# Optimization experiments

Measured on AMD Instinct MI355X. Metric: run time of the kernel, lower is better.

Reference implementation:

```python
import jax, jax.numpy as jnp
import numpy as np

B, N, E, H = 2, 4096, 1024, 16
HD = E // H                      # head_dim = 64
R = 8                            # LoRA rank
LORA_SCALE = 16.0 / R            # alpha / r = 2.0
BUCKET_SIZES = (256, 64, 16)


def setup_inputs() -> dict:
    key = jax.random.key(0)
    ks = jax.random.split(key, 24)
    inp = {"x": jax.random.normal(ks[0], (B, N, E), jnp.float32)}
    inp["wb_coarse"] = jax.random.randint(ks[1], (B, N), 0, 16)
    inp["wb_mid"] = jax.random.randint(ks[2], (B, N), 0, 64)
    inp["wb_fine"] = jax.random.randint(ks[3], (B, N), 0, 256)
    i = 4
    for name in ("q", "k", "v", "o"):
        inp[f"W{name}"] = jax.random.normal(ks[i], (E, E), jnp.float32) / np.sqrt(E); i += 1
        inp[f"b{name}"] = jax.random.normal(ks[i], (E,), jnp.float32) * 0.01; i += 1
        inp[f"A{name}"] = jax.random.normal(ks[i], (R, E), jnp.float32) / np.sqrt(E); i += 1
        inp[f"B{name}"] = jax.random.normal(ks[i], (E, R), jnp.float32) * 0.01; i += 1
    return inp


def _lora(x, W, b, A, Bm):
    # F.linear(x, W, b) + scale * x @ A.T @ B.T   (dropout=0 in eval)
    return x @ W.T + b + LORA_SCALE * ((x @ A.T) @ Bm.T)


def _chunked_attn(q, k, v, bidx, C):
    # q,k,v: [BH, N, D]; bidx: [BH, N] int; C: chunk size (divides N)
    BH, Nn, D = q.shape
    sidx = jnp.argsort(bidx, axis=1)
    uidx = jnp.argsort(sidx, axis=1)
    g = lambda t, i: jnp.take_along_axis(t, i[..., None], axis=1)
    qs, ks_, vs = g(q, sidx), g(k, sidx), g(v, sidx)
    nc = Nn // C
    qs = qs.reshape(BH, nc, C, D)
    ks_ = ks_.reshape(BH, nc, C, D)
    vs = vs.reshape(BH, nc, C, D)
    # previous chunk (look-back of one chunk); chunk 0 has no previous -> masked
    k_prev = jnp.concatenate([jnp.zeros_like(ks_[:, :1]), ks_[:, :-1]], axis=1)
    v_prev = jnp.concatenate([jnp.zeros_like(vs[:, :1]), vs[:, :-1]], axis=1)
    k_cat = jnp.concatenate([k_prev, ks_], axis=2)   # [BH, nc, 2C, D]
    v_cat = jnp.concatenate([v_prev, vs], axis=2)
    scores = jnp.einsum('bncd,bnkd->bnck', qs, k_cat) / jnp.sqrt(jnp.asarray(D, qs.dtype))
    # mask look-back keys for chunk 0 (torch path attends only within chunk 0)
    chunk_ids = jnp.arange(nc)[:, None, None]        # [nc,1,1]
    key_pos = jnp.arange(2 * C)[None, None, :]       # [1,1,2C]
    neg = jnp.finfo(scores.dtype).min
    scores = jnp.where((chunk_ids == 0) & (key_pos < C), neg, scores)
    attn = jax.nn.softmax(scores, axis=-1)
    out = jnp.einsum('bnck,bnkd->bncd', attn, v_cat).reshape(BH, Nn, D)
    return jnp.take_along_axis(out, uidx[..., None], axis=1)


def reference(x, wb_coarse, wb_mid, wb_fine,
              Wq, bq, Aq, Bq, Wk, bk, Ak, Bk,
              Wv, bv, Av, Bv, Wo, bo, Ao, Bo):
    q = _lora(x, Wq, bq, Aq, Bq)
    k = _lora(x, Wk, bk, Ak, Bk)
    v = _lora(x, Wv, bv, Av, Bv)
    to_heads = lambda t: t.reshape(B, N, H, HD).transpose(0, 2, 1, 3).reshape(B * H, N, HD)
    qh, kh, vh = to_heads(q), to_heads(k), to_heads(v)
    expand = lambda w: jnp.broadcast_to(w[:, None, :], (B, H, N)).reshape(B * H, N)
    wbs = (expand(wb_coarse), expand(wb_mid), expand(wb_fine))
    outs = (_chunked_attn(qh, kh, vh, wbs[0], BUCKET_SIZES[0])
            + _chunked_attn(qh, kh, vh, wbs[1], BUCKET_SIZES[1])
            + _chunked_attn(qh, kh, vh, wbs[2], BUCKET_SIZES[2])) / 3.0
    outs = outs.reshape(B, H, N, HD).transpose(0, 2, 1, 3).reshape(B, N, E)
    return _lora(outs, Wo, bo, Ao, Bo)
```

## Files before the change

kernel.cpp:

```cpp
#include <hip/hip_runtime.h>
#include <cstdint>
#include <cstddef>

#define BDIM 2
#define NTOK 4096
#define EDIM 1024
#define HEADS 16
#define HDIM 64
#define MROWS (BDIM * NTOK)

typedef unsigned short u16;
typedef __attribute__((ext_vector_type(8))) short bf16x8;
typedef __attribute__((ext_vector_type(8))) unsigned short u16x8;
typedef __attribute__((ext_vector_type(4))) float f32x4;

#define MFMA(a, b, c) __builtin_amdgcn_mfma_f32_16x16x32_bf16(a, b, c, 0, 0, 0)
#define BAR() asm volatile("s_barrier" ::: "memory")
#define SETPRIO(p) __builtin_amdgcn_s_setprio(p)

__device__ inline void split2(float x, u16& h, u16& l) {
    union { float f; unsigned u; } a;
    a.f = x;
    unsigned uh = a.u + 0x7fff + ((a.u >> 16) & 1);
    h = (u16)(uh >> 16);
    union { unsigned u; float f; } hf; hf.u = (unsigned)h << 16;
    a.f = x - hf.f;
    unsigned ul = a.u + 0x7fff + ((a.u >> 16) & 1);
    l = (u16)(ul >> 16);
}

__device__ inline u16 bf16rne(float x) {
    union { float f; unsigned u; } a; a.f = x;
    unsigned r = a.u + 0x7fff + ((a.u >> 16) & 1);
    return (u16)(r >> 16);
}

#define GLL(gp, lp) __builtin_amdgcn_global_load_lds( \
    (const __attribute__((address_space(1))) unsigned*)(gp), \
    (__attribute__((address_space(3))) unsigned*)(lp), 16, 0, 0)

__global__ __launch_bounds__(256) void prep_kernel(
    const float* __restrict__ x, u16* __restrict__ xh, u16* __restrict__ xl,
    const int* __restrict__ w0, const int* __restrict__ w1,
    const int* __restrict__ w2, int* __restrict__ sidx,
    const float* __restrict__ W0, const float* __restrict__ A0, const float* __restrict__ B0,
    const float* __restrict__ W1, const float* __restrict__ A1, const float* __restrict__ B1,
    const float* __restrict__ W2, const float* __restrict__ A2, const float* __restrict__ B2,
    const float* __restrict__ W3, const float* __restrict__ A3, const float* __restrict__ B3,
    u16* __restrict__ dh0, u16* __restrict__ dl0,
    u16* __restrict__ dh1, u16* __restrict__ dl1,
    u16* __restrict__ dh2, u16* __restrict__ dl2,
    u16* __restrict__ dh3, u16* __restrict__ dl3)
{
    __shared__ int sb[NTOK];
    __shared__ int cnt[32][256];
    __shared__ int gb[256];
    int bid = blockIdx.x;
    int t = threadIdx.x;

    if (bid < 6) {
        int by = bid >> 1, bx = bid & 1;
        const int* srcs[3] = {w0, w1, w2};
        const int* w = srcs[by] + bx * NTOK;
        int* outp = sidx + ((int)by * BDIM + (int)bx) * NTOK;

        for (int i = t; i < NTOK; i += 256) sb[i] = w[i];
        for (int i = t; i < 32 * 256; i += 256) ((int*)cnt)[i] = 0;
        __syncthreads();

        int g = t >> 3;
#pragma unroll
        for (int e = 0; e < 16; ++e)
            atomicAdd(&cnt[g][sb[g * 128 + (t & 7) + 8 * e]], 1);
        __syncthreads();

        int run = 0;
#pragma unroll
        for (int gg = 0; gg < 32; ++gg) {
            int c = cnt[gg][t];
            cnt[gg][t] = run;
            run += c;
        }
        gb[t] = run;
        __syncthreads();
        if (t == 0) {
            int acc = 0;
            for (int v = 0; v < 256; ++v) { int c = gb[v]; gb[v] = acc; acc += c; }
        }
        __syncthreads();
        for (int i = t; i < 32 * 256; i += 256) {
            int v = i & 255, gg = i >> 8;
            cnt[gg][v] += gb[v];
        }
        __syncthreads();

        if (t < 32) {
            int base = t * 128;
            for (int e = 0; e < 128; ++e) {
                int v = sb[base + e];
                int p = cnt[t][v]++;
                outp[p] = base + e;
            }
        }
    } else if (bid < 8198) {
        int idx = (bid - 6) * 256 + t;
        float4 v = ((const float4*)x)[idx];
        ushort4 h, l;
        split2(v.x, h.x, l.x);
        split2(v.y, h.y, l.y);
        split2(v.z, h.z, l.z);
        split2(v.w, h.w, l.w);
        ((ushort4*)xh)[idx] = h;
        ((ushort4*)xl)[idx] = l;
    } else {
        int wid = bid - 8198;
        int s = wid >> 12, bx = wid & 4095;
        const float* W = (s == 0) ? W0 : (s == 1) ? W1 : (s == 2) ? W2 : W3;
        const float* A = (s == 0) ? A0 : (s == 1) ? A1 : (s == 2) ? A2 : A3;
        const float* Bm = (s == 0) ? B0 : (s == 1) ? B1 : (s == 2) ? B2 : B3;
        u16* dh = (s == 0) ? dh0 : (s == 1) ? dh1 : (s == 2) ? dh2 : dh3;
        u16* dl = (s == 0) ? dl0 : (s == 1) ? dl1 : (s == 2) ? dl2 : dl3;

        int idx = bx * 256 + t;
        int o = idx >> 10, i = idx & 1023;
        float sum = 0.f;
#pragma unroll
        for (int r = 0; r < 8; ++r) sum += Bm[o * 8 + r] * A[r * 1024 + i];
        float w = W[idx] + 2.0f * sum;
        u16 h, l;
        split2(w, h, l);
        dh[idx] = h; dl[idx] = l;
    }
}

__global__ __launch_bounds__(256) void sumsplit3_kernel(
    const float* __restrict__ A, const float* __restrict__ B,
    const float* __restrict__ Cc, u16* __restrict__ dh, u16* __restrict__ dl)
{
    int idx = blockIdx.x * 256 + threadIdx.x;
    float4 a = ((const float4*)A)[idx];
    float4 b = ((const float4*)B)[idx];
    float4 c = ((const float4*)Cc)[idx];
    float v[4] = {(a.x + b.x) + c.x, (a.y + b.y) + c.y,
                  (a.z + b.z) + c.z, (a.w + b.w) + c.w};
    ushort4 h, l;
    split2(v[0], h.x, l.x);
    split2(v[1], h.y, l.y);
    split2(v[2], h.z, l.z);
    split2(v[3], h.w, l.w);
    ((ushort4*)dh)[idx] = h;
    ((ushort4*)dl)[idx] = l;
}

__global__ __launch_bounds__(256) void split_kernel(
    const float* __restrict__ src, u16* __restrict__ dh, u16* __restrict__ dl)
{
    int idx = blockIdx.x * 256 + threadIdx.x;
    float4 v = ((const float4*)src)[idx];
    ushort4 h, l;
    split2(v.x, h.x, l.x);
    split2(v.y, h.y, l.y);
    split2(v.z, h.z, l.z);
    split2(v.w, h.w, l.w);
    ((ushort4*)dh)[idx] = h;
    ((ushort4*)dl)[idx] = l;
}

__global__ __launch_bounds__(512, 2) void gemm_qkv_kernel(
    const u16* __restrict__ Xh, const u16* __restrict__ Xl,
    const u16* __restrict__ Wh, const u16* __restrict__ Wl,
    const u16* __restrict__ Wvh,
    const float* __restrict__ bq, const float* __restrict__ bk,
    const float* __restrict__ bv,
    u16* __restrict__ qh, u16* __restrict__ ql,
    u16* __restrict__ kh, u16* __restrict__ kl, u16* __restrict__ vh)
{
    __shared__ __align__(16) unsigned char smem[147456];
    u16* lds = (u16*)smem;
    int t = threadIdx.x;
    int lane = t & 63, wave = t >> 6;
    int bid = blockIdx.x;

    if (bid < 256) {
        int wg = (bid & 7) * 32 + (bid >> 3);
        int bx = wg & 7, by = wg >> 3;
        int m0 = by * 256, nc0 = bx * 128;

        int lrow = lane & 15, lq = lane >> 4;
        size_t aoff = (size_t)(m0 + wave * 32 + lrow) * EDIM + lq * 8;
        size_t boff = (size_t)(nc0 + wave * 16 + lrow) * EDIM + lq * 8;
        int slabA = wave * 2;
        int sA0 = (wave >> 1) * 4;
        int sB0 = (wave & 1) * 4;
        f32x4 acc[4][4] = {};

#pragma unroll
        for (int tt = 0; tt < 2; ++tt) {
            u16* sbuf = lds + tt * 12288;
            int kk = tt * 32;
            GLL(Xh + aoff + kk,             sbuf + (slabA + 0) * 512);
            GLL(Xh + aoff + kk + 16 * EDIM, sbuf + (slabA + 1) * 512);
            GLL(Wvh + boff + kk,            sbuf + 8192 + wave * 512);
        }
        asm volatile("s_waitcnt vmcnt(3)" ::: "memory");
        BAR();

        for (int t32 = 0; t32 < 32; ++t32) {
            u16* rb = lds + (t32 % 3) * 12288;
            u16* sbuf = lds + ((t32 + 2) % 3) * 12288;
            bool pf = (t32 + 2) < 32;
            int kn = (t32 + 2) * 32;

            bf16x8 bhf[4];
#pragma unroll
            for (int j = 0; j < 4; ++j)
                bhf[j] = *(const bf16x8*)(rb + 8192 + (sB0 + j) * 512 + lane * 8);
            bf16x8 a0 = *(const bf16x8*)(rb + (sA0 + 0) * 512 + lane * 8);
            bf16x8 a1 = *(const bf16x8*)(rb + (sA0 + 1) * 512 + lane * 8);
            if (pf) {
                GLL(Xh + aoff + kn,             sbuf + (slabA + 0) * 512);
                GLL(Xh + aoff + kn + 16 * EDIM, sbuf + (slabA + 1) * 512);
            }
            BAR();
            SETPRIO(1);
#pragma unroll
            for (int j = 0; j < 4; ++j) {
                acc[0][j] = MFMA(a0, bhf[j], acc[0][j]);
                acc[1][j] = MFMA(a1, bhf[j], acc[1][j]);
            }
            SETPRIO(0);
            BAR();

            bf16x8 a2 = *(const bf16x8*)(rb + (sA0 + 2) * 512 + lane * 8);
            bf16x8 a3 = *(const bf16x8*)(rb + (sA0 + 3) * 512 + lane * 8);
            if (pf) GLL(Wvh + boff + kn, sbuf + 8192 + wave * 512);
            BAR();
            SETPRIO(1);
#pragma unroll
            for (int j = 0; j < 4; ++j) {
                acc[2][j] = MFMA(a2, bhf[j], acc[2][j]);
                acc[3][j] = MFMA(a3, bhf[j], acc[3][j]);
            }
            SETPRIO(0);
            if (pf) asm volatile("s_waitcnt vmcnt(3)" ::: "memory");
            else    asm volatile("s_waitcnt vmcnt(0)" ::: "memory");
            BAR();
        }

        int wm = (wave >> 1) * 64, wn = (wave & 1) * 64;
        int q4 = lane >> 4, l16 = lane & 15;
        int cb = nc0 + wn;
        float bj[4];
#pragma unroll
        for (int j = 0; j < 4; ++j) bj[j] = bv[cb + j * 16 + l16];
        float* repw = (float*)smem + wave * 2176;
        int r8 = lane >> 3, c8 = lane & 7;
#pragma unroll
        for (int gph = 0; gph < 2; ++gph) {
#pragma unroll
            for (int ii = 0; ii < 2; ++ii)
#pragma unroll
                for (int j = 0; j < 4; ++j)
#pragma unroll
                    for (int r = 0; r < 4; ++r)
                        repw[(ii * 16 + q4 * 4 + r) * 68 + j * 16 + l16] =
                            acc[gph * 2 + ii][j][r] + bj[j];
#pragma unroll
            for (int rg = 0; rg < 4; ++rg) {
                int lr = rg * 8 + r8;
                float4 f0 = *(float4*)(repw + lr * 68 + c8 * 8);
                float4 f1 = *(float4*)(repw + lr * 68 + c8 * 8 + 4);
                float fa[8] = {f0.x, f0.y, f0.z, f0.w, f1.x, f1.y, f1.z, f1.w};
                size_t off = (size_t)(m0 + wm + gph * 32 + lr) * EDIM + cb + c8 * 8;
                u16x8 hv;
#pragma unroll
                for (int e = 0; e < 8; ++e) hv[e] = bf16rne(fa[e]);
                *(u16x8*)(vh + off) = hv;
            }
        }
    } else {
        const int PA_h = 0, PA_l = 8192, PB_h = 16384, PB_l = 20480;
        int qidx = bid - 256;
        int wg = (qidx & 7) * 64 + (qidx >> 3);
        int bx = wg & 15, by = wg >> 4;
        int m0 = by * 256, n0 = bx * 128;

        int lrow = lane & 15, lq = lane >> 4;
        size_t aoff = (size_t)(m0 + wave * 32 + lrow) * EDIM + lq * 8;
        size_t boff = (size_t)(n0 + wave * 16 + lrow) * EDIM + lq * 8;
        int slabA = wave * 2;
        int sA0 = (wave >> 1) * 4;
        int sB0 = (wave & 1) * 4;
        f32x4 acc[4][4] = {};

#pragma unroll
        for (int tt = 0; tt < 2; ++tt) {
            u16* sbuf = lds + tt * 24576;
            int kk = tt * 32;
            GLL(Xh + aoff + kk,             sbuf + PA_h + (slabA + 0) * 512);
            GLL(Xh + aoff + kk + 16 * EDIM, sbuf + PA_h + (slabA + 1) * 512);
            GLL(Xl + aoff + kk,             sbuf + PA_l + (slabA + 0) * 512);
            GLL(Xl + aoff + kk + 16 * EDIM, sbuf + PA_l + (slabA + 1) * 512);
            GLL(Wh + boff + kk, sbuf + PB_h + wave * 512);
            GLL(Wl + boff + kk, sbuf + PB_l + wave * 512);
        }
        asm volatile("s_waitcnt vmcnt(6)" ::: "memory");
        BAR();

        for (int t32 = 0; t32 < 32; ++t32) {
            u16* rb = lds + (t32 % 3) * 24576;
            u16* sbuf = lds + ((t32 + 2) % 3) * 24576;
            bool pf = (t32 + 2) < 32;
            int kn = (t32 + 2) * 32;
            bf16x8 bhf[4], blf[4];
#pragma unroll
            for (int p = 0; p < 4; ++p) {
                if (p == 0) {
#pragma unroll
                    for (int j = 0; j < 4; ++j) {
                        bhf[j] = *(const bf16x8*)(rb + PB_h + (sB0 + j) * 512 + lane * 8);
                        blf[j] = *(const bf16x8*)(rb + PB_l + (sB0 + j) * 512 + lane * 8);
                    }
                }
                bf16x8 aph = *(const bf16x8*)(rb + PA_h + (sA0 + p) * 512 + lane * 8);
                bf16x8 apl = *(const bf16x8*)(rb + PA_l + (sA0 + p) * 512 + lane * 8);
                if (pf) {
                    if (p == 0) {
                        GLL(Xh + aoff + kn,             sbuf + PA_h + (slabA + 0) * 512);
                        GLL(Xh + aoff + kn + 16 * EDIM, sbuf + PA_h + (slabA + 1) * 512);
                    } else if (p == 1) {
                        GLL(Xl + aoff + kn,             sbuf + PA_l + (slabA + 0) * 512);
                        GLL(Xl + aoff + kn + 16 * EDIM, sbuf + PA_l + (slabA + 1) * 512);
                    } else if (p == 2) {
                        GLL(Wh + boff + kn, sbuf + PB_h + wave * 512);
                        GLL(Wl + boff + kn, sbuf + PB_l + wave * 512);
                    }
                }
                BAR();
                SETPRIO(1);
#pragma unroll
                for (int j = 0; j < 4; ++j) {
                    acc[p][j] = MFMA(aph, bhf[j], acc[p][j]);
                    acc[p][j] = MFMA(aph, blf[j], acc[p][j]);
                    acc[p][j] = MFMA(apl, bhf[j], acc[p][j]);
                }
                SETPRIO(0);
                if (p == 3) {
                    if (pf) asm volatile("s_waitcnt vmcnt(6)" ::: "memory");
                    else    asm volatile("s_waitcnt vmcnt(0)" ::: "memory");
                }
                BAR();
            }
        }

        int proj = n0 >> 10;
        const float* bias = proj ? bk : bq;
        u16* ohp = proj ? kh : qh;
        u16* olp = proj ? kl : ql;
        int wm = (wave >> 1) * 64, wn = (wave & 1) * 64;
        int q4 = lane >> 4, l16 = lane & 15;
        int cb = (n0 & 1023) + wn;
        float bj[4];
#pragma unroll
        for (int j = 0; j < 4; ++j) bj[j] = bias[cb + j * 16 + l16];
        float* repw = (float*)smem + wave * 2176;
        int r8 = lane >> 3, c8 = lane & 7;
#pragma unroll
        for (int gph = 0; gph < 2; ++gph) {
#pragma unroll
            for (int ii = 0; ii < 2; ++ii)
#pragma unroll
                for (int j = 0; j < 4; ++j)
#pragma unroll
                    for (int r = 0; r < 4; ++r)
                        repw[(ii * 16 + q4 * 4 + r) * 68 + j * 16 + l16] =
                            acc[gph * 2 + ii][j][r] + bj[j];
#pragma unroll
            for (int rg = 0; rg < 4; ++rg) {
                int lr = rg * 8 + r8;
                float4 f0 = *(float4*)(repw + lr * 68 + c8 * 8);
                float4 f1 = *(float4*)(repw + lr * 68 + c8 * 8 + 4);
                float fa[8] = {f0.x, f0.y, f0.z, f0.w, f1.x, f1.y, f1.z, f1.w};
                size_t off = (size_t)(m0 + wm + gph * 32 + lr) * EDIM + cb + c8 * 8;
                u16x8 hv, lv;
#pragma unroll
                for (int e = 0; e < 8; ++e) {
                    float v = fa[e];
                    if (proj == 0) v *= 0.125f;
                    u16 hh, ll;
                    split2(v, hh, ll);
                    hv[e] = hh; lv[e] = ll;
                }
                *(u16x8*)(ohp + off) = hv;
                *(u16x8*)(olp + off) = lv;
            }
        }
    }
}

__global__ __launch_bounds__(512, 2) void gemm_o_kernel(
    const u16* __restrict__ Xh, const u16* __restrict__ Xl,
    const u16* __restrict__ Wh, const u16* __restrict__ Wl,
    const float* __restrict__ bias, float* __restrict__ Y)
{
    __shared__ __align__(16) unsigned char smem[147456];
    u16* lds = (u16*)smem;
    const int PA_h = 0, PA_l = 8192, PB_h = 16384, PB_l = 20480;

    int t = threadIdx.x;
    int lane = t & 63, wave = t >> 6;
    int bid = blockIdx.x;
    int wg = (bid & 7) * 32 + (bid >> 3);
    int bx = wg & 7, by = wg >> 3;
    int m0 = by * 256, n0 = bx * 128;

    int lrow = lane & 15, lq = lane >> 4;
    size_t aoff = (size_t)(m0 + wave * 32 + lrow) * EDIM + lq * 8;
    size_t boff = (size_t)(n0 + wave * 16 + lrow) * EDIM + lq * 8;
    int slabA = wave * 2;
    int sA0 = (wave >> 1) * 4;
    int sB0 = (wave & 1) * 4;
    f32x4 acc[4][4] = {};

#pragma unroll
    for (int tt = 0; tt < 2; ++tt) {
        u16* sbuf = lds + tt * 24576;
        int kk = tt * 32;
        GLL(Xh + aoff + kk,             sbuf + PA_h + (slabA + 0) * 512);
        GLL(Xh + aoff + kk + 16 * EDIM, sbuf + PA_h + (slabA + 1) * 512);
        GLL(Xl + aoff + kk,             sbuf + PA_l + (slabA + 0) * 512);
        GLL(Xl + aoff + kk + 16 * EDIM, sbuf + PA_l + (slabA + 1) * 512);
        GLL(Wh + boff + kk, sbuf + PB_h + wave * 512);
        GLL(Wl + boff + kk, sbuf + PB_l + wave * 512);
    }
    asm volatile("s_waitcnt vmcnt(6)" ::: "memory");
    BAR();

    for (int t32 = 0; t32 < 32; ++t32) {
        u16* rb = lds + (t32 % 3) * 24576;
        u16* sbuf = lds + ((t32 + 2) % 3) * 24576;
        bool pf = (t32 + 2) < 32;
        int kn = (t32 + 2) * 32;
        bf16x8 bhf[4], blf[4];
#pragma unroll
        for (int p = 0; p < 4; ++p) {
            if (p == 0) {
#pragma unroll
                for (int j = 0; j < 4; ++j) {
                    bhf[j] = *(const bf16x8*)(rb + PB_h + (sB0 + j) * 512 + lane * 8);
                    blf[j] = *(const bf16x8*)(rb + PB_l + (sB0 + j) * 512 + lane * 8);
                }
            }
            bf16x8 aph = *(const bf16x8*)(rb + PA_h + (sA0 + p) * 512 + lane * 8);
            bf16x8 apl = *(const bf16x8*)(rb + PA_l + (sA0 + p) * 512 + lane * 8);
            if (pf) {
                if (p == 0) {
                    GLL(Xh + aoff + kn,             sbuf + PA_h + (slabA + 0) * 512);
                    GLL(Xh + aoff + kn + 16 * EDIM, sbuf + PA_h + (slabA + 1) * 512);
                } else if (p == 1) {
                    GLL(Xl + aoff + kn,             sbuf + PA_l + (slabA + 0) * 512);
                    GLL(Xl + aoff + kn + 16 * EDIM, sbuf + PA_l + (slabA + 1) * 512);
                } else if (p == 2) {
                    GLL(Wh + boff + kn, sbuf + PB_h + wave * 512);
                    GLL(Wl + boff + kn, sbuf + PB_l + wave * 512);
                }
            }
            BAR();
            SETPRIO(1);
#pragma unroll
            for (int j = 0; j < 4; ++j) {
                acc[p][j] = MFMA(aph, bhf[j], acc[p][j]);
                acc[p][j] = MFMA(aph, blf[j], acc[p][j]);
                acc[p][j] = MFMA(apl, bhf[j], acc[p][j]);
            }
            SETPRIO(0);
            if (p == 3) {
                if (pf) asm volatile("s_waitcnt vmcnt(6)" ::: "memory");
                else    asm volatile("s_waitcnt vmcnt(0)" ::: "memory");
            }
            BAR();
        }
    }

    int wm = (wave >> 1) * 64, wn = (wave & 1) * 64;
    int col_in = lane & 15, rquad = lane >> 4;
#pragma unroll
    for (int j = 0; j < 4; ++j) {
        int col = n0 + wn + j * 16 + col_in;
        float bvv = bias[col];
#pragma unroll
        for (int i = 0; i < 4; ++i) {
            int mbase = m0 + wm + i * 16 + rquad * 4;
#pragma unroll
            for (int r = 0; r < 4; ++r)
                Y[(size_t)(mbase + r) * EDIM + col] = acc[i][j][r] + bvv;
        }
    }
}

template <int MODE>
__global__ __launch_bounds__(256, 3) void attn_mfma_kernel(
    const u16* __restrict__ Qh, const u16* __restrict__ Ql,
    const u16* __restrict__ Kh, const u16* __restrict__ Kl,
    const u16* __restrict__ Vh, const int* __restrict__ sidx_base, int zofs,
    float* __restrict__ out0, float* __restrict__ out1, float* __restrict__ out2,
    u16* __restrict__ osh, u16* __restrict__ osl)
{
    __shared__ u16 KfH[2][4096], KfL[2][4096];
    __shared__ u16 VL[64 * 72];
    __shared__ u16 PbH[4 * 2 * 16 * 40];

    int bx_, bh_, bz_;
    if (MODE == 0 && gridDim.z == 3) {
        int lid = blockIdx.x + (blockIdx.y << 5) + (blockIdx.z << 10);
        int xcd = lid & 7, j = lid >> 3;
        bh_ = xcd + 8 * (j / 96);
        int rem = j % 96;
        bz_ = rem >> 5;
        bx_ = rem & 31;
    } else {
        bx_ = blockIdx.x; bh_ = blockIdx.y; bz_ = blockIdx.z;
    }

    int sidx_i = bz_ + zofs;
    int lgC = 8 - 2 * sidx_i;
    const int* sxb = sidx_base + sidx_i * BDIM * NTOK;
    float* out = (sidx_i == 0) ? out0 : (sidx_i == 1) ? out1 : out2;

    int t = threadIdx.x;
    int lane = t & 63, wave = t >> 6;
    int quad = lane >> 4, l16 = lane & 15;
    int b = bh_ >> 4, h = bh_ & 15;
    int p0 = bx_ * 128;
    sxb += b * NTOK;

    int ptile[2], ws_[2], we_[2];
    bf16x8 qhf[2][2], qlf[2][2];
#pragma unroll
    for (int tq = 0; tq < 2; ++tq) {
        ptile[tq] = p0 + wave * 32 + tq * 16;
        int c = ptile[tq] >> lgC;
        ws_[tq] = (c > 0) ? (c - 1) << lgC : 0;
        we_[tq] = (c + 1) << lgC;
        int qrow = sxb[ptile[tq] + l16];
        size_t rb = (size_t)(b * NTOK + qrow) * EDIM + h * HDIM + quad * 8;
#pragma unroll
        for (int kk = 0; kk < 2; ++kk) {
            qhf[tq][kk] = *(const bf16x8*)(Qh + rb + kk * 32);
            qlf[tq][kk] = *(const bf16x8*)(Ql + rb + kk * 32);
        }
    }

    f32x4 oacc[2][4] = {};
    float lpart[2][4] = {};
    float mrun[2] = {-1e30f, -1e30f};

    int c0 = p0 >> lgC, c1 = (p0 + 127) >> lgC;
    int kmin = (c0 > 0) ? (c0 - 1) << lgC : 0;
    int kmax = (c1 + 1) << lgC;
    int nsteps = (kmax - kmin + 63) >> 6;

    {
        int tok = sxb[min(kmin + wave * 16 + l16, NTOK - 1)];
        size_t rb = (size_t)(b * NTOK + tok) * EDIM + h * HDIM + quad * 8;
        GLL(Kh + rb,      &KfH[0][(wave * 2 + 0) * 512]);
        GLL(Kh + rb + 32, &KfH[0][(wave * 2 + 1) * 512]);
        GLL(Kl + rb,      &KfL[0][(wave * 2 + 0) * 512]);
        GLL(Kl + rb + 32, &KfL[0][(wave * 2 + 1) * 512]);
        bf16x8 vreg[2];
#pragma unroll
        for (int it = 0; it < 2; ++it) {
            int c = it * 256 + t;
            int key = c & 63, dg = c >> 6;
            int tok2 = sxb[min(kmin + key, NTOK - 1)];
            vreg[it] = *(const bf16x8*)(Vh + (size_t)(b * NTOK + tok2) * EDIM + h * HDIM + dg * 8);
        }
#pragma unroll
        for (int it = 0; it < 2; ++it) {
            int c = it * 256 + t;
            int key = c & 63, dg = c >> 6;
#pragma unroll
            for (int e = 0; e < 8; ++e)
                VL[(dg * 8 + e) * 72 + key] = (u16)vreg[it][e];
        }
        asm volatile("s_waitcnt vmcnt(0)" ::: "memory");
        __syncthreads();
    }

    int pb = 0;
    for (int s = 0; s < nsteps; ++s) {
        int ks = kmin + s * 64;
        int nk = min(64, kmax - ks);
        bool pf = (s + 1) < nsteps;
        bf16x8 vreg[2];
        if (pf) {
            int ks2 = ks + 64;
            int tok = sxb[min(ks2 + wave * 16 + l16, NTOK - 1)];
            size_t rb = (size_t)(b * NTOK + tok) * EDIM + h * HDIM + quad * 8;
            GLL(Kh + rb,      &KfH[pb ^ 1][(wave * 2 + 0) * 512]);
            GLL(Kh + rb + 32, &KfH[pb ^ 1][(wave * 2 + 1) * 512]);
            GLL(Kl + rb,      &KfL[pb ^ 1][(wave * 2 + 0) * 512]);
            GLL(Kl + rb + 32, &KfL[pb ^ 1][(wave * 2 + 1) * 512]);
#pragma unroll
            for (int it = 0; it < 2; ++it) {
                int c = it * 256 + t;
                int key = c & 63, dg = c >> 6;
                int tok2 = sxb[min(ks2 + key, NTOK - 1)];
                vreg[it] = *(const bf16x8*)(Vh + (size_t)(b * NTOK + tok2) * EDIM + h * HDIM + dg * 8);
            }
        }

        int jlo0 = max(ks, ws_[0]) - ks, jhi0 = min(ks + nk, we_[0]) - ks;
        int jlo1 = max(ks, ws_[1]) - ks, jhi1 = min(ks + nk, we_[1]) - ks;
        bool e0 = jlo0 < jhi0, e1 = jlo1 < jhi1;
        if (e0 || e1) {
            int glo = e0 ? (e1 ? min(jlo0, jlo1) : jlo0) : jlo1;
            int ghi = e0 ? (e1 ? max(jhi0, jhi1) : jhi0) : jhi1;
            const u16* kfh = &KfH[pb][0];
            const u16* kfl = &KfL[pb][0];

            for (int g0 = glo & ~31; g0 < ghi; g0 += 32) {
                int s0i = g0 >> 4;
                int s1i = min(s0i + 1, 3);
                bf16x8 kh0[2], kl0[2], kh1[2], kl1[2];
#pragma unroll
                for (int kk = 0; kk < 2; ++kk) {
                    kh0[kk] = *(const bf16x8*)(kfh + ((s0i * 2 + kk) * 64 + lane) * 8);
                    kl0[kk] = *(const bf16x8*)(kfl + ((s0i * 2 + kk) * 64 + lane) * 8);
                    kh1[kk] = *(const bf16x8*)(kfh + ((s1i * 2 + kk) * 64 + lane) * 8);
                    kl1[kk] = *(const bf16x8*)(kfl + ((s1i * 2 + kk) * 64 + lane) * 8);
                }
#pragma unroll
                for (int tq = 0; tq < 2; ++tq) {
                    int jl = tq ? jlo1 : jlo0, jh = tq ? jhi1 : jhi0;
                    bool v0 = (g0 >= jl) && (g0 < jh);
                    bool v1 = (g0 + 16 >= jl) && (g0 + 16 < jh);
                    if (!v0 && !v1) continue;
                    f32x4 sa = {0.f, 0.f, 0.f, 0.f}, sb2 = {0.f, 0.f, 0.f, 0.f};
                    SETPRIO(1);
                    if (v0) {
                        sa = MFMA(qhf[tq][0], kh0[0], sa);
                        sa = MFMA(qhf[tq][0], kl0[0], sa);
                        sa = MFMA(qlf[tq][0], kh0[0], sa);
                        sa = MFMA(qhf[tq][1], kh0[1], sa);
                        sa = MFMA(qhf[tq][1], kl0[1], sa);
                        sa = MFMA(qlf[tq][1], kh0[1], sa);
                    }
                    if (v1) {
                        sb2 = MFMA(qhf[tq][0], kh1[0], sb2);
                        sb2 = MFMA(qhf[tq][0], kl1[0], sb2);
                        sb2 = MFMA(qlf[tq][0], kh1[0], sb2);
                        sb2 = MFMA(qhf[tq][1], kh1[1], sb2);
                        sb2 = MFMA(qhf[tq][1], kl1[1], sb2);
                        sb2 = MFMA(qlf[tq][1], kh1[1], sb2);
                    }
                    SETPRIO(0);
                    float smax = -1e30f;
                    if (v0) smax = fmaxf(smax, fmaxf(fmaxf(sa[0], sa[1]), fmaxf(sa[2], sa[3])));
                    if (v1) smax = fmaxf(smax, fmaxf(fmaxf(sb2[0], sb2[1]), fmaxf(sb2[2], sb2[3])));
                    smax = fmaxf(smax, __shfl_xor(smax, 1));
                    smax = fmaxf(smax, __shfl_xor(smax, 2));
                    smax = fmaxf(smax, __shfl_xor(smax, 4));
                    smax = fmaxf(smax, __shfl_xor(smax, 8));
                    float mold = mrun[tq];
                    float mnew = mold;
                    if (smax > mold + 8.0f) {
                        mnew = smax;
                        mrun[tq] = mnew;
                        float alpha = __expf(mold - mnew);
#pragma unroll
                        for (int r = 0; r < 4; ++r) lpart[tq][r] *= alpha;
#pragma unroll
                        for (int dt = 0; dt < 4; ++dt) {
                            oacc[tq][dt][0] *= alpha; oacc[tq][dt][1] *= alpha;
                            oacc[tq][dt][2] *= alpha; oacc[tq][dt][3] *= alpha;
                        }
                    }
                    u16* pbh = PbH + wave * 1280 + tq * 640;
#pragma unroll
                    for (int r = 0; r < 4; ++r) {
                        float pa = v0 ? __expf(sa[r] - mnew) : 0.f;
                        float pbv = v1 ? __expf(sb2[r] - mnew) : 0.f;
                        lpart[tq][r] += pa + pbv;
                        pbh[(quad * 4 + r) * 40 + l16] = bf16rne(pa);
                        pbh[(quad * 4 + r) * 40 + 16 + l16] = bf16rne(pbv);
                    }
                    bf16x8 ph = *(const bf16x8*)(pbh + l16 * 40 + quad * 8);
                    int kh2 = g0 >> 5;
                    SETPRIO(1);
#pragma unroll
                    for (int dt = 0; dt < 4; ++dt) {
                        bf16x8 vv = *(const bf16x8*)(VL + (dt * 16 + l16) * 72 + kh2 * 32 + quad * 8);
                        oacc[tq][dt] = MFMA(ph, vv, oacc[tq][dt]);
                    }
                    SETPRIO(0);
                }
            }
        }

        asm volatile("s_waitcnt vmcnt(0)" ::: "memory");
        __syncthreads();
        if (pf) {
#pragma unroll
            for (int it = 0; it < 2; ++it) {
                int c = it * 256 + t;
                int key = c & 63, dg = c >> 6;
#pragma unroll
                for (int e = 0; e < 8; ++e)
                    VL[(dg * 8 + e) * 72 + key] = (u16)vreg[it][e];
            }
        }
        __syncthreads();
        pb ^= 1;
    }

#pragma unroll
    for (int tq = 0; tq < 2; ++tq) {
        float inv[4];
#pragma unroll
        for (int r = 0; r < 4; ++r) {
            float v = lpart[tq][r];
            v += __shfl_xor(v, 1);
            v += __shfl_xor(v, 2);
            v += __shfl_xor(v, 4);
            v += __shfl_xor(v, 8);
            inv[r] = 1.0f / (3.0f * v);
        }
#pragma unroll
        for (int r = 0; r < 4; ++r) {
            int tok = sxb[ptile[tq] + quad * 4 + r];
            size_t base = (size_t)(b * NTOK + tok) * EDIM + h * HDIM + l16;
            if (MODE == 2) {
#pragma unroll
                for (int dt = 0; dt < 4; ++dt) {
                    float v = out[base + dt * 16] + oacc[tq][dt][r] * inv[r];
                    u16 hh, ll;
                    split2(v, hh, ll);
                    osh[base + dt * 16] = hh;
                    osl[base + dt * 16] = ll;
                }
            } else if (MODE == 1) {
#pragma unroll
                for (int dt = 0; dt < 4; ++dt)
                    out[base + dt * 16] += oacc[tq][dt][r] * inv[r];
            } else {
#pragma unroll
                for (int dt = 0; dt < 4; ++dt)
                    out[base + dt * 16] = oacc[tq][dt][r] * inv[r];
            }
        }
    }
}

extern "C" void kernel_launch(void* const* d_in, const int* in_sizes, int n_in,
                              void* d_out, int out_size, void* d_ws, size_t ws_size,
                              hipStream_t stream)
{
    const float* x   = (const float*)d_in[0];
    const int*   wbc = (const int*)d_in[1];
    const int*   wbm = (const int*)d_in[2];
    const int*   wbf = (const int*)d_in[3];
    const float* Wq = (const float*)d_in[4],  *bq = (const float*)d_in[5];
    const float* Aq = (const float*)d_in[6],  *Bq = (const float*)d_in[7];
    const float* Wk = (const float*)d_in[8],  *bk = (const float*)d_in[9];
    const float* Ak = (const float*)d_in[10], *Bk = (const float*)d_in[11];
    const float* Wv = (const float*)d_in[12], *bv = (const float*)d_in[13];
    const float* Av = (const float*)d_in[14], *Bv = (const float*)d_in[15];
    const float* Wo = (const float*)d_in[16], *bo = (const float*)d_in[17];
    const float* Ao = (const float*)d_in[18], *Bo = (const float*)d_in[19];

    const size_t EE  = (size_t)EDIM * EDIM;
    const size_t BNE = (size_t)MROWS * EDIM;

    char* wsb = (char*)d_ws;
    float* ab = (float*)wsb;                        wsb += BNE * 4;
    u16* xh = (u16*)wsb;                            wsb += BNE * 2;
    u16* xl = (u16*)wsb;                            wsb += BNE * 2;
    u16* qh = (u16*)wsb;                            wsb += BNE * 2;
    u16* ql = (u16*)wsb;                            wsb += BNE * 2;
    u16* kh = (u16*)wsb;                            wsb += BNE * 2;
    u16* kl = (u16*)wsb;                            wsb += BNE * 2;
    u16* vh = (u16*)wsb;                            wsb += BNE * 2;
    u16* wh_all = (u16*)wsb;                        wsb += 3 * EE * 2;
    u16* wl_all = (u16*)wsb;                        wsb += 3 * EE * 2;
    u16* woh = (u16*)wsb;                           wsb += EE * 2;
    u16* wol = (u16*)wsb;                           wsb += EE * 2;
    int* sidx = (int*)wsb;                          wsb += 3 * BDIM * NTOK * 4;
    float* abC = (float*)wsb;
    size_t need3 = (size_t)(wsb - (char*)d_ws) + BNE * 4;
    bool merged = (ws_size >= need3);

    prep_kernel<<<24582, 256, 0, stream>>>(
        x, xh, xl, wbc, wbm, wbf, sidx,
        Wq, Aq, Bq, Wk, Ak, Bk, Wv, Av, Bv, Wo, Ao, Bo,
        wh_all + 0 * EE, wl_all + 0 * EE,
        wh_all + 1 * EE, wl_all + 1 * EE,
        wh_all + 2 * EE, wl_all + 2 * EE,
        woh, wol);

    gemm_qkv_kernel<<<768, 512, 0, stream>>>(
        xh, xl, wh_all, wl_all, wh_all + 2 * EE,
        bq, bk, bv, qh, ql, kh, kl, vh);

    if (merged) {
        float* abB = (float*)xh;
        dim3 ga3(NTOK / 128, BDIM * HEADS, 3);
        attn_mfma_kernel<0><<<ga3, 256, 0, stream>>>(
            qh, ql, kh, kl, vh, sidx, 0, ab, abB, abC, nullptr, nullptr);
        sumsplit3_kernel<<<BNE / 1024, 256, 0, stream>>>(ab, abB, abC, qh, ql);
        gemm_o_kernel<<<256, 512, 0, stream>>>(qh, ql, woh, wol, bo, (float*)d_out);
    } else {
        dim3 ga(NTOK / 128, BDIM * HEADS);
        attn_mfma_kernel<0><<<ga, 256, 0, stream>>>(
            qh, ql, kh, kl, vh, sidx, 0, ab, ab, ab, nullptr, nullptr);
        attn_mfma_kernel<1><<<ga, 256, 0, stream>>>(
            qh, ql, kh, kl, vh, sidx, 1, ab, ab, ab, nullptr, nullptr);
        attn_mfma_kernel<2><<<ga, 256, 0, stream>>>(
            qh, ql, kh, kl, vh, sidx, 2, ab, ab, ab, xh, xl);
        gemm_o_kernel<<<256, 512, 0, stream>>>(xh, xl, woh, wol, bo, (float*)d_out);
    }
}
```

Before: 469.2 us.

## Drop K double-buffering and shrink LDS to raise attention kernel occupancy

Removes the double-buffered K tiles and the per-query-tile softmax staging buffer, cutting LDS use per block, and raises launch bounds from 3 to 5 blocks per CU. The next K/V tile is now loaded after the compute step, between barriers, so global loads no longer overlap with MFMA work inside a block. The intent is to hide that memory latency through more resident blocks instead. The two query tiles now share one P staging buffer per wave, which is safe only because each wave finishes with it before reusing it, and the tighter register budget may cause spills.

```diff
diff --git a/kernel.cpp b/kernel.cpp
--- a/kernel.cpp
+++ b/kernel.cpp
@@ -499,16 +499,16 @@
 }
 
 template <int MODE>
-__global__ __launch_bounds__(256, 3) void attn_mfma_kernel(
+__global__ __launch_bounds__(256, 5) void attn_mfma_kernel(
     const u16* __restrict__ Qh, const u16* __restrict__ Ql,
     const u16* __restrict__ Kh, const u16* __restrict__ Kl,
     const u16* __restrict__ Vh, const int* __restrict__ sidx_base, int zofs,
     float* __restrict__ out0, float* __restrict__ out1, float* __restrict__ out2,
     u16* __restrict__ osh, u16* __restrict__ osl)
 {
-    __shared__ u16 KfH[2][4096], KfL[2][4096];
+    __shared__ u16 KfH[4096], KfL[4096];
     __shared__ u16 VL[64 * 72];
-    __shared__ u16 PbH[4 * 2 * 16 * 40];
+    __shared__ u16 PbH[4 * 16 * 40];
 
     int bx_, bh_, bz_;
     if (MODE == 0 && gridDim.z == 3) {
@@ -563,10 +563,10 @@
     {
         int tok = sxb[min(kmin + wave * 16 + l16, NTOK - 1)];
         size_t rb = (size_t)(b * NTOK + tok) * EDIM + h * HDIM + quad * 8;
-        GLL(Kh + rb,      &KfH[0][(wave * 2 + 0) * 512]);
-        GLL(Kh + rb + 32, &KfH[0][(wave * 2 + 1) * 512]);
-        GLL(Kl + rb,      &KfL[0][(wave * 2 + 0) * 512]);
-        GLL(Kl + rb + 32, &KfL[0][(wave * 2 + 1) * 512]);
+        GLL(Kh + rb,      &KfH[(wave * 2 + 0) * 512]);
+        GLL(Kh + rb + 32, &KfH[(wave * 2 + 1) * 512]);
+        GLL(Kl + rb,      &KfL[(wave * 2 + 0) * 512]);
+        GLL(Kl + rb + 32, &KfL[(wave * 2 + 1) * 512]);
         bf16x8 vreg[2];
 #pragma unroll
         for (int it = 0; it < 2; ++it) {
@@ -587,28 +587,10 @@
         __syncthreads();
     }
 
-    int pb = 0;
     for (int s = 0; s < nsteps; ++s) {
         int ks = kmin + s * 64;
         int nk = min(64, kmax - ks);
         bool pf = (s + 1) < nsteps;
-        bf16x8 vreg[2];
-        if (pf) {
-            int ks2 = ks + 64;
-            int tok = sxb[min(ks2 + wave * 16 + l16, NTOK - 1)];
-            size_t rb = (size_t)(b * NTOK + tok) * EDIM + h * HDIM + quad * 8;
-            GLL(Kh + rb,      &KfH[pb ^ 1][(wave * 2 + 0) * 512]);
-            GLL(Kh + rb + 32, &KfH[pb ^ 1][(wave * 2 + 1) * 512]);
-            GLL(Kl + rb,      &KfL[pb ^ 1][(wave * 2 + 0) * 512]);
-            GLL(Kl + rb + 32, &KfL[pb ^ 1][(wave * 2 + 1) * 512]);
-#pragma unroll
-            for (int it = 0; it < 2; ++it) {
-                int c = it * 256 + t;
-                int key = c & 63, dg = c >> 6;
-                int tok2 = sxb[min(ks2 + key, NTOK - 1)];
-                vreg[it] = *(const bf16x8*)(Vh + (size_t)(b * NTOK + tok2) * EDIM + h * HDIM + dg * 8);
-            }
-        }
 
         int jlo0 = max(ks, ws_[0]) - ks, jhi0 = min(ks + nk, we_[0]) - ks;
         int jlo1 = max(ks, ws_[1]) - ks, jhi1 = min(ks + nk, we_[1]) - ks;
@@ -616,8 +598,6 @@
         if (e0 || e1) {
             int glo = e0 ? (e1 ? min(jlo0, jlo1) : jlo0) : jlo1;
             int ghi = e0 ? (e1 ? max(jhi0, jhi1) : jhi0) : jhi1;
-            const u16* kfh = &KfH[pb][0];
-            const u16* kfl = &KfL[pb][0];
 
             for (int g0 = glo & ~31; g0 < ghi; g0 += 32) {
                 int s0i = g0 >> 4;
@@ -625,10 +605,10 @@
                 bf16x8 kh0[2], kl0[2], kh1[2], kl1[2];
 #pragma unroll
                 for (int kk = 0; kk < 2; ++kk) {
-                    kh0[kk] = *(const bf16x8*)(kfh + ((s0i * 2 + kk) * 64 + lane) * 8);
-                    kl0[kk] = *(const bf16x8*)(kfl + ((s0i * 2 + kk) * 64 + lane) * 8);
-                    kh1[kk] = *(const bf16x8*)(kfh + ((s1i * 2 + kk) * 64 + lane) * 8);
-                    kl1[kk] = *(const bf16x8*)(kfl + ((s1i * 2 + kk) * 64 + lane) * 8);
+                    kh0[kk] = *(const bf16x8*)(KfH + ((s0i * 2 + kk) * 64 + lane) * 8);
+                    kl0[kk] = *(const bf16x8*)(KfL + ((s0i * 2 + kk) * 64 + lane) * 8);
+                    kh1[kk] = *(const bf16x8*)(KfH + ((s1i * 2 + kk) * 64 + lane) * 8);
+                    kl1[kk] = *(const bf16x8*)(KfL + ((s1i * 2 + kk) * 64 + lane) * 8);
                 }
 #pragma unroll
                 for (int tq = 0; tq < 2; ++tq) {
@@ -676,7 +656,7 @@
                             oacc[tq][dt][2] *= alpha; oacc[tq][dt][3] *= alpha;
                         }
                     }
-                    u16* pbh = PbH + wave * 1280 + tq * 640;
+                    u16* pbh = PbH + wave * 640;
 #pragma unroll
                     for (int r = 0; r < 4; ++r) {
                         float pa = v0 ? __expf(sa[r] - mnew) : 0.f;
@@ -698,20 +678,34 @@
             }
         }
 
-        asm volatile("s_waitcnt vmcnt(0)" ::: "memory");
         __syncthreads();
         if (pf) {
+            int ks2 = ks + 64;
+            int tok = sxb[min(ks2 + wave * 16 + l16, NTOK - 1)];
+            size_t rb = (size_t)(b * NTOK + tok) * EDIM + h * HDIM + quad * 8;
+            GLL(Kh + rb,      &KfH[(wave * 2 + 0) * 512]);
+            GLL(Kh + rb + 32, &KfH[(wave * 2 + 1) * 512]);
+            GLL(Kl + rb,      &KfL[(wave * 2 + 0) * 512]);
+            GLL(Kl + rb + 32, &KfL[(wave * 2 + 1) * 512]);
+            bf16x8 vreg[2];
 #pragma unroll
             for (int it = 0; it < 2; ++it) {
                 int c = it * 256 + t;
                 int key = c & 63, dg = c >> 6;
+                int tok2 = sxb[min(ks2 + key, NTOK - 1)];
+                vreg[it] = *(const bf16x8*)(Vh + (size_t)(b * NTOK + tok2) * EDIM + h * HDIM + dg * 8);
+            }
+#pragma unroll
+            for (int it = 0; it < 2; ++it) {
+                int c = it * 256 + t;
+                int key = c & 63, dg = c >> 6;
 #pragma unroll
                 for (int e = 0; e < 8; ++e)
                     VL[(dg * 8 + e) * 72 + key] = (u16)vreg[it][e];
             }
+            asm volatile("s_waitcnt vmcnt(0)" ::: "memory");
         }
         __syncthreads();
-        pb ^= 1;
     }
 
 #pragma unroll
```

After: 779.8 us. 66.2% more time.
